# Kernel optimization log

Hardware: AMD Instinct MI355X
Metric: run time of the kernel (lower is better)

Reference implementation:

```python
import jax, jax.numpy as jnp
import numpy as np

B, N, D_ROI = 16, 128, 12544   # images, detections/image, C*roi*roi = 256*7*7
HID, PARTS = 128, 22
DTH, CTH = 50.0, 0.8           # dist / cosine thresholds
EPS = 1e-12


def setup_inputs() -> dict:
    key = jax.random.key(0)
    ks = jax.random.split(key, 6)
    d_in = D_ROI + 2
    fv = jax.random.normal(ks[0], (B, N, D_ROI), jnp.float32)
    ctr = jax.random.uniform(ks[1], (B, N, 2), jnp.float32) * 640.0  # xyxyn*640 centers
    W1 = jax.random.normal(ks[2], (d_in, HID), jnp.float32) / np.float32(np.sqrt(d_in))
    b1 = jnp.zeros((HID,), jnp.float32)
    W2 = jax.random.normal(ks[3], (HID, HID), jnp.float32) / np.float32(np.sqrt(HID))
    b2 = jnp.zeros((HID,), jnp.float32)
    Wc = jax.random.normal(ks[4], (HID, PARTS), jnp.float32) / np.float32(np.sqrt(HID))
    bc = jnp.zeros((PARTS,), jnp.float32)
    return {"fv": fv, "ctr": ctr, "W1": W1, "b1": b1, "W2": W2, "b2": b2, "Wc": Wc, "bc": bc}


def _adjacency(fv, ctr):
    """Per-image graph build: (cdist < dth) | (cosine > cth), + PyG self-loop."""
    # squared pairwise distance (compare against DTH^2; avoids sqrt at 0)
    d2 = jnp.sum((ctr[:, :, None, :] - ctr[:, None, :, :]) ** 2, axis=-1)  # [B,N,N]
    fvn = fv / jnp.maximum(jnp.linalg.norm(fv, axis=-1, keepdims=True), EPS)
    cos = jnp.einsum("bnd,bmd->bnm", fvn, fvn)                              # [B,N,N]
    A = ((d2 < DTH * DTH) | (cos > CTH)).astype(jnp.float32)
    # GCNConv(add_self_loops=True) adds weight-1 self loops on top of existing edges
    A = A + jnp.eye(N, dtype=jnp.float32)
    deg = jnp.sum(A, axis=-1)                                               # >= 2 on diag
    dinv = jax.lax.rsqrt(deg)
    return dinv[:, :, None] * A * dinv[:, None, :]                          # D^-1/2 A D^-1/2


def reference(fv, ctr, W1, b1, W2, b2, Wc, bc):
    A_hat = _adjacency(fv, ctr)                         # [B,N,N]
    x = jnp.concatenate([fv, ctr], axis=-1)             # [B,N,D_roi+2]
    h = jax.nn.relu(jnp.einsum("bnm,bmh->bnh", A_hat, x @ W1) + b1)
    h = jax.nn.relu(jnp.einsum("bnm,bmh->bnh", A_hat, h @ W2) + b2)
    hg = jnp.mean(h, axis=1)                            # global_mean_pool per image
    logits = hg @ Wc + bc                               # [B, PARTS]
    return logits
```

## Files before the change

kernel.cpp:

```cpp
#include <hip/hip_runtime.h>
#include <stdint.h>

#define DROI   12544
#define BIMG   16
#define NDET   128
#define NHID   128

typedef __bf16 bf16x8 __attribute__((ext_vector_type(8)));
typedef float  f32x4  __attribute__((ext_vector_type(4)));

__device__ __forceinline__ unsigned pk2(float a, float b){
  unsigned ua = __float_as_uint(a), ub = __float_as_uint(b);
  ua = (ua + 0x7fffu + ((ua >> 16) & 1u)) >> 16;
  ub = (ub + 0x7fffu + ((ub >> 16) & 1u)) >> 16;
  return ua | (ub << 16);
}
__device__ __forceinline__ unsigned short bf1(float a){
  unsigned ua = __float_as_uint(a);
  return (unsigned short)((ua + 0x7fffu + ((ua >> 16) & 1u)) >> 16);
}
__device__ __forceinline__ f32x4 mfma16(bf16x8 a, bf16x8 b, f32x4 c){
  return __builtin_amdgcn_mfma_f32_16x16x32_bf16(a, b, c, 0, 0, 0);
}
__device__ __forceinline__ void gl_lds16(const void* g, void* l){
  __builtin_amdgcn_global_load_lds(
      (const __attribute__((address_space(1))) unsigned int*)g,
      (__attribute__((address_space(3))) unsigned int*)l, 16, 0, 0);
}
__device__ __forceinline__ bf16x8 ldfrag128(const short* base, int row, int bo){
  const char* p = (const char*)base + row * 128 + (bo ^ ((row & 7) << 4));
  return *(const bf16x8*)p;
}
__device__ __forceinline__ bf16x8 ldfrag256(const short* base, int row, int bo){
  const char* p = (const char*)base + row * 256 + (bo ^ ((row & 7) << 4));
  return *(const bf16x8*)p;
}

__global__ __launch_bounds__(256) void k0_wt(const float* __restrict__ W1,
                                             unsigned short* __restrict__ Wt){
  __shared__ float tile[64][133];
  const int t  = threadIdx.x;
  const int k0 = blockIdx.x * 64;
  const int r0 = t >> 5;
  const int c4 = (t & 31) * 4;
#pragma unroll
  for (int i = 0; i < 8; ++i){
    int r = r0 + i * 8;
    float4 v = *(const float4*)(W1 + (long)(k0 + r) * NHID + c4);
    tile[r][c4+0] = v.x; tile[r][c4+1] = v.y; tile[r][c4+2] = v.z; tile[r][c4+3] = v.w;
  }
  __syncthreads();
  const int h  = t >> 1;
  const int kc = (t & 1) * 32;
  unsigned* dst = (unsigned*)(Wt + (long)h * DROI + k0 + kc);
#pragma unroll
  for (int kk = 0; kk < 32; kk += 2)
    dst[kk >> 1] = pk2(tile[kc + kk][h], tile[kc + kk + 1][h]);
}

template<int SK>
__global__ __launch_bounds__(256, 2) void k1_main(const float* __restrict__ fv,
    const unsigned short* __restrict__ Wt, float* __restrict__ part){
  constexpr int KC = DROI / SK;
  constexpr int NT = KC / 64;
  __shared__ __align__(16) short lsA[2][8192];
  __shared__ __align__(16) short lsB[2][8192];
  const int tid  = threadIdx.x;
  const int wave = tid >> 6, lane = tid & 63;
  const int s = blockIdx.x, b = blockIdx.y;
  const int kbase = s * KC;

  f32x4 acc[4][8];
  {
    f32x4 z = {0.f, 0.f, 0.f, 0.f};
#pragma unroll
    for (int m = 0; m < 4; ++m)
#pragma unroll
      for (int c = 0; c < 8; ++c) acc[m][c] = z;
  }

  const int r0   = tid >> 4;
  const int colf = (tid & 15) * 4;
  const float* fvt = fv + (long)(b * NDET + r0) * DROI + kbase + colf;
  const int hh  = lane >> 3;
  const int seg = (lane & 7) ^ hh;

  float4 stg[8];
#pragma unroll
  for (int j = 0; j < 4; ++j){
    int call = wave * 4 + j;
    int h = call * 8 + hh;
    const char* g = (const char*)Wt + (long)h * (DROI * 2) + (long)kbase * 2 + seg * 16;
    gl_lds16(g, (char*)lsB[0] + call * 1024);
  }
#pragma unroll
  for (int i = 0; i < 8; ++i) stg[i] = *(const float4*)(fvt + (long)i * 16 * DROI);
  {
    char* basep = (char*)lsA[0];
#pragma unroll
    for (int i = 0; i < 8; ++i){
      int r = r0 + i * 16;
      uint2 w; w.x = pk2(stg[i].x, stg[i].y); w.y = pk2(stg[i].z, stg[i].w);
      *(uint2*)(basep + r * 128 + ((colf * 2) ^ ((r & 7) << 4))) = w;
    }
  }
  __syncthreads();

  const int outw = wave >> 1;
  const int mh   = wave & 1;
  const int lq   = lane & 15;
  int buf = 0;
  for (int t = 0; t < NT; ++t){
    const int nt = t + 1;
    if (nt < NT){
#pragma unroll
      for (int j = 0; j < 4; ++j){
        int call = wave * 4 + j;
        int h = call * 8 + hh;
        const char* g = (const char*)Wt + (long)h * (DROI * 2)
                      + (long)(kbase + nt * 64) * 2 + seg * 16;
        gl_lds16(g, (char*)lsB[buf ^ 1] + call * 1024);
      }
      const float* fp = fvt + nt * 64;
#pragma unroll
      for (int i = 0; i < 8; ++i) stg[i] = *(const float4*)(fp + (long)i * 16 * DROI);
    }
    const short* A  = lsA[buf];
    const short* Bs = outw ? lsB[buf] : lsA[buf];
#pragma unroll
    for (int kk = 0; kk < 2; ++kk){
      const int bo = kk * 64 + (lane >> 4) * 16;
      bf16x8 am[4];
#pragma unroll
      for (int m = 0; m < 4; ++m)
        am[m] = ldfrag128(A, mh * 64 + m * 16 + lq, bo);
#pragma unroll
      for (int cb = 0; cb < 8; ++cb){
        bf16x8 bb = ldfrag128(Bs, cb * 16 + lq, bo);
#pragma unroll
        for (int m = 0; m < 4; ++m)
          acc[m][cb] = mfma16(am[m], bb, acc[m][cb]);
      }
    }
    if (nt < NT){
      char* basep = (char*)lsA[buf ^ 1];
#pragma unroll
      for (int i = 0; i < 8; ++i){
        int r = r0 + i * 16;
        uint2 w; w.x = pk2(stg[i].x, stg[i].y); w.y = pk2(stg[i].z, stg[i].w);
        *(uint2*)(basep + r * 128 + ((colf * 2) ^ ((r & 7) << 4))) = w;
      }
    }
    __syncthreads();
    buf ^= 1;
  }

  float* dst = part + ((long)s * 32 + b * 2 + outw) * 16384;
#pragma unroll
  for (int m = 0; m < 4; ++m){
    const int R0 = mh * 64 + m * 16 + (lane >> 4) * 4;
#pragma unroll
    for (int cb = 0; cb < 8; ++cb){
#pragma unroll
      for (int i = 0; i < 4; ++i)
        dst[(R0 + i) * 128 + cb * 16 + lq] = acc[m][cb][i];
    }
  }
}

template<int SK>
__global__ __launch_bounds__(256) void k_reduce(const float4* __restrict__ part4,
                                                float4* __restrict__ fin4){
  const int e = blockIdx.x * 256 + threadIdx.x;
  float4 s = {0.f, 0.f, 0.f, 0.f};
#pragma unroll
  for (int k = 0; k < SK; ++k){
    float4 p = part4[(long)k * 131072 + e];
    s.x += p.x; s.y += p.y; s.z += p.z; s.w += p.w;
  }
  fin4[e] = s;
}

__global__ __launch_bounds__(256, 1) void k2f(const float* __restrict__ fin,
    const float* __restrict__ ctr, const float* __restrict__ W1,
    const float* __restrict__ b1, const float* __restrict__ W2,
    const float* __restrict__ b2, const float* __restrict__ Wc,
    const float* __restrict__ bc, float* __restrict__ out){
  __shared__ __align__(16) short Ah[16384];
  __shared__ __align__(16) short Bu[16384];
  __shared__ __align__(16) short Cu[16384];
  __shared__ float sm2[256];
  const int b   = blockIdx.x;
  const int tid = threadIdx.x;
  const float* G = fin + (long)b * 32768;
  const float* Y = G + 16384;

  if (tid < 128){
    float g = G[tid * 129];
    sm2[tid] = 1.0f / fmaxf(sqrtf(g), 1e-12f);
  }
  __syncthreads();

  const int   i   = tid >> 1;
  const int   jb  = (tid & 1) * 64;
  const float invni = sm2[i];
  const float cxi = ctr[(b * 128 + i) * 2 + 0];
  const float cyi = ctr[(b * 128 + i) * 2 + 1];
  unsigned m0 = 0, m1 = 0;
  int degloc = 0;
  for (int j4 = 0; j4 < 64; j4 += 4){
    float4 g4 = *(const float4*)(G + i * 128 + jb + j4);
    float gg[4] = {g4.x, g4.y, g4.z, g4.w};
#pragma unroll
    for (int u = 0; u < 4; ++u){
      int j = jb + j4 + u;
      float cs = gg[u] * invni * sm2[j];
      float dx = cxi - ctr[(b * 128 + j) * 2 + 0];
      float dy = cyi - ctr[(b * 128 + j) * 2 + 1];
      float d2 = dx * dx + dy * dy;
      if (d2 < 2500.0f || cs > 0.8f){
        int bp = j4 + u;
        if (bp < 32) m0 |= (1u << bp); else m1 |= (1u << (bp - 32));
        ++degloc;
      }
    }
  }
  if (i >= jb && i < jb + 64) ++degloc;
  int degfull = degloc + __shfl_xor(degloc, 1);
  if ((tid & 1) == 0) sm2[128 + i] = rsqrtf((float)degfull);
  __syncthreads();

  {
    const float dinvi = sm2[128 + i];
    char* AhB = (char*)Ah;
    for (int jp = 0; jp < 64; jp += 2){
      int j0 = jb + jp, j1 = j0 + 1;
      float a0 = (((jp   < 32) ? ((m0 >> jp)       & 1u) : ((m1 >> (jp - 32))     & 1u)) ? 1.f : 0.f);
      float a1 = (((jp+1 < 32) ? ((m0 >> (jp + 1)) & 1u) : ((m1 >> (jp + 1 - 32)) & 1u)) ? 1.f : 0.f);
      if (i == j0) a0 += 1.f;
      if (i == j1) a1 += 1.f;
      float v0 = dinvi * a0 * sm2[128 + j0];
      float v1 = dinvi * a1 * sm2[128 + j1];
      int bo = j0 * 2;
      *(unsigned*)(AhB + i * 256 + (bo ^ ((i & 7) << 4))) = pk2(v0, v1);
    }
  }

  const int c     = tid & 127;
  const int khalf = tid >> 7;
  {
    char* WB = (char*)Cu;
    for (int k8 = khalf * 64; k8 < khalf * 64 + 64; k8 += 8){
      float f[8];
#pragma unroll
      for (int u = 0; u < 8; ++u) f[u] = W2[(k8 + u) * 128 + c];
      uint4 w;
      w.x = pk2(f[0], f[1]); w.y = pk2(f[2], f[3]);
      w.z = pk2(f[4], f[5]); w.w = pk2(f[6], f[7]);
      int bo = k8 * 2;
      *(uint4*)(WB + c * 256 + (bo ^ ((c & 7) << 4))) = w;
    }
  }
  {
    const float w1a = W1[(long)12544 * NHID + c];
    const float w1b = W1[(long)12545 * NHID + c];
    char* YtB = (char*)Bu;
    for (int k8 = khalf * 64; k8 < khalf * 64 + 64; k8 += 8){
      float f[8];
#pragma unroll
      for (int u = 0; u < 8; ++u){
        int k = k8 + u;
        f[u] = Y[k * 128 + c] + ctr[(b*128 + k)*2 + 0] * w1a + ctr[(b*128 + k)*2 + 1] * w1b;
      }
      uint4 w;
      w.x = pk2(f[0], f[1]); w.y = pk2(f[2], f[3]);
      w.z = pk2(f[4], f[5]); w.w = pk2(f[6], f[7]);
      int bo = k8 * 2;
      *(uint4*)(YtB + c * 256 + (bo ^ ((c & 7) << 4))) = w;
    }
  }
  __syncthreads();

  const int wave = tid >> 6, lane = tid & 63;
  const int lq = lane & 15;
  f32x4 acc[2][8];
  f32x4 z4 = {0.f, 0.f, 0.f, 0.f};

#pragma unroll
  for (int r = 0; r < 2; ++r)
#pragma unroll
    for (int cc = 0; cc < 8; ++cc) acc[r][cc] = z4;
#pragma unroll
  for (int ks = 0; ks < 4; ++ks){
    const int bo = ks * 64 + (lane >> 4) * 16;
    bf16x8 a0 = ldfrag256(Ah, (wave*2+0)*16 + lq, bo);
    bf16x8 a1 = ldfrag256(Ah, (wave*2+1)*16 + lq, bo);
#pragma unroll
    for (int cb = 0; cb < 8; ++cb){
      bf16x8 bb = ldfrag256(Bu, cb*16 + lq, bo);
      acc[0][cb] = mfma16(a0, bb, acc[0][cb]);
      acc[1][cb] = mfma16(a1, bb, acc[1][cb]);
    }
  }
  __syncthreads();
  {
    char* BuB = (char*)Bu;
#pragma unroll
    for (int rb = 0; rb < 2; ++rb){
      const int R0 = wave*32 + rb*16 + (lane >> 4)*4;
#pragma unroll
      for (int cb = 0; cb < 8; ++cb){
        const int C = cb*16 + lq;
        const float bb1 = b1[C];
#pragma unroll
        for (int u = 0; u < 4; ++u){
          float v = fmaxf(acc[rb][cb][u] + bb1, 0.f);
          int row = R0 + u;
          *(unsigned short*)(BuB + row * 256 + ((C * 2) ^ ((row & 7) << 4))) = bf1(v);
        }
      }
    }
  }
  __syncthreads();

#pragma unroll
  for (int r = 0; r < 2; ++r)
#pragma unroll
    for (int cc = 0; cc < 8; ++cc) acc[r][cc] = z4;
#pragma unroll
  for (int ks = 0; ks < 4; ++ks){
    const int bo = ks * 64 + (lane >> 4) * 16;
    bf16x8 a0 = ldfrag256(Bu, (wave*2+0)*16 + lq, bo);
    bf16x8 a1 = ldfrag256(Bu, (wave*2+1)*16 + lq, bo);
#pragma unroll
    for (int cb = 0; cb < 8; ++cb){
      bf16x8 bb = ldfrag256(Cu, cb*16 + lq, bo);
      acc[0][cb] = mfma16(a0, bb, acc[0][cb]);
      acc[1][cb] = mfma16(a1, bb, acc[1][cb]);
    }
  }
  __syncthreads();
  {
    char* BuB = (char*)Bu;
#pragma unroll
    for (int rb = 0; rb < 2; ++rb){
      const int R0 = wave*32 + rb*16 + (lane >> 4)*4;
#pragma unroll
      for (int cb = 0; cb < 8; ++cb){
        const int C = cb*16 + lq;
#pragma unroll
        for (int u = 0; u < 4; ++u){
          int k = R0 + u;
          *(unsigned short*)(BuB + C * 256 + ((k * 2) ^ ((C & 7) << 4))) = bf1(acc[rb][cb][u]);
        }
      }
    }
  }
  __syncthreads();

#pragma unroll
  for (int r = 0; r < 2; ++r)
#pragma unroll
    for (int cc = 0; cc < 8; ++cc) acc[r][cc] = z4;
#pragma unroll
  for (int ks = 0; ks < 4; ++ks){
    const int bo = ks * 64 + (lane >> 4) * 16;
    bf16x8 a0 = ldfrag256(Ah, (wave*2+0)*16 + lq, bo);
    bf16x8 a1 = ldfrag256(Ah, (wave*2+1)*16 + lq, bo);
#pragma unroll
    for (int cb = 0; cb < 8; ++cb){
      bf16x8 bb = ldfrag256(Bu, cb*16 + lq, bo);
      acc[0][cb] = mfma16(a0, bb, acc[0][cb]);
      acc[1][cb] = mfma16(a1, bb, acc[1][cb]);
    }
  }
  float colp[8];
#pragma unroll
  for (int cb = 0; cb < 8; ++cb){
    const int C = cb*16 + lq;
    const float bb2 = b2[C];
    float sum = 0.f;
#pragma unroll
    for (int rb = 0; rb < 2; ++rb)
#pragma unroll
      for (int u = 0; u < 4; ++u)
        sum += fmaxf(acc[rb][cb][u] + bb2, 0.f);
    colp[cb] = sum;
  }
#pragma unroll
  for (int cb = 0; cb < 8; ++cb){
    float v = colp[cb];
    v += __shfl_xor(v, 16);
    v += __shfl_xor(v, 32);
    colp[cb] = v;
  }
  __syncthreads();
  float* hgp = (float*)Cu;
  if ((lane >> 4) == 0){
#pragma unroll
    for (int cb = 0; cb < 8; ++cb)
      hgp[wave * 128 + cb * 16 + lane] = colp[cb];
  }
  __syncthreads();
  float* hg = hgp + 512;
  if (tid < 128)
    hg[tid] = (hgp[tid] + hgp[128 + tid] + hgp[256 + tid] + hgp[384 + tid]) * (1.0f / 128.0f);
  __syncthreads();
  if (tid < 22){
    float a2 = bc[tid];
    for (int h = 0; h < 128; ++h) a2 += hg[h] * Wc[h * 22 + tid];
    out[b * 22 + tid] = a2;
  }
}

extern "C" void kernel_launch(void* const* d_in, const int* in_sizes, int n_in,
                              void* d_out, int out_size, void* d_ws, size_t ws_size,
                              hipStream_t stream){
  (void)in_sizes; (void)n_in; (void)out_size;
  const float* fv  = (const float*)d_in[0];
  const float* ctr = (const float*)d_in[1];
  const float* W1  = (const float*)d_in[2];
  const float* b1  = (const float*)d_in[3];
  const float* W2  = (const float*)d_in[4];
  const float* b2  = (const float*)d_in[5];
  const float* Wc  = (const float*)d_in[6];
  const float* bc  = (const float*)d_in[7];
  char* ws = (char*)d_ws;
  float* out = (float*)d_out;

  const unsigned long SZ_WT = (unsigned long)NHID * DROI * 2;
  const unsigned long SZ_FIN = (unsigned long)BIMG * 2 * 16384 * 4;

  const unsigned long need28 = SZ_WT + 28UL * 2097152UL + SZ_FIN;
  const bool big = (ws_size >= need28);
  const int SK = big ? 28 : 14;

  unsigned short* Wt   = (unsigned short*)(ws);
  float*          part = (float*)(ws + SZ_WT);
  float*          fin  = (float*)(ws + SZ_WT + (unsigned long)SK * 2097152UL);

  k0_wt<<<dim3(DROI / 64), dim3(256), 0, stream>>>(W1, Wt);
  if (big){
    k1_main<28><<<dim3(28, BIMG), dim3(256), 0, stream>>>(fv, Wt, part);
    k_reduce<28><<<dim3(512), dim3(256), 0, stream>>>((const float4*)part, (float4*)fin);
  } else {
    k1_main<14><<<dim3(14, BIMG), dim3(256), 0, stream>>>(fv, Wt, part);
    k_reduce<14><<<dim3(512), dim3(256), 0, stream>>>((const float4*)part, (float4*)fin);
  }
  k2f<<<dim3(BIMG), dim3(256), 0, stream>>>(fin, ctr, W1, b1, W2, b2, Wc, bc, out);
}
```

Baseline: 70.97 us.

## Use 512-thread GEMM blocks, bf16 split-K partials, transposed Y layout in reduce

The main Gram/projection kernel moves to 512 threads per block, with each wave owning 32 rows instead of 64. fv is loaded as contiguous 64-byte row segments per thread. Split-K partials are stored packed as bf16 in the raw MFMA fragment order, which halves the partial-sum traffic. The reduce kernel unscrambles that order and writes Y transposed, so the final kernel can read rows with float4 loads and keeps centers in shared memory. The trade-off is extra bf16 rounding error in the partial sums before they are accumulated, which could affect the cosine-threshold adjacency decisions.

Result: faster. 65.35 us (-7.9%).

```diff
diff --git a/kernel.cpp b/kernel.cpp
--- a/kernel.cpp
+++ b/kernel.cpp
@@ -59,8 +59,8 @@
 }
 
 template<int SK>
-__global__ __launch_bounds__(256, 2) void k1_main(const float* __restrict__ fv,
-    const unsigned short* __restrict__ Wt, float* __restrict__ part){
+__global__ __launch_bounds__(512, 4) void k1_main(const float* __restrict__ fv,
+    const unsigned short* __restrict__ Wt, unsigned* __restrict__ part){
   constexpr int KC = DROI / SK;
   constexpr int NT = KC / 64;
   __shared__ __align__(16) short lsA[2][8192];
@@ -70,52 +70,54 @@
   const int s = blockIdx.x, b = blockIdx.y;
   const int kbase = s * KC;
 
-  f32x4 acc[4][8];
+  f32x4 acc[2][8];
   {
     f32x4 z = {0.f, 0.f, 0.f, 0.f};
 #pragma unroll
-    for (int m = 0; m < 4; ++m)
+    for (int m = 0; m < 2; ++m)
 #pragma unroll
       for (int c = 0; c < 8; ++c) acc[m][c] = z;
   }
 
-  const int r0   = tid >> 4;
-  const int colf = (tid & 15) * 4;
+  const int r0   = tid >> 2;
+  const int colf = (tid & 3) * 16;
   const float* fvt = fv + (long)(b * NDET + r0) * DROI + kbase + colf;
   const int hh  = lane >> 3;
   const int seg = (lane & 7) ^ hh;
 
-  float4 stg[8];
-#pragma unroll
-  for (int j = 0; j < 4; ++j){
-    int call = wave * 4 + j;
+  float4 stg[4];
+#pragma unroll
+  for (int j = 0; j < 2; ++j){
+    int call = wave * 2 + j;
     int h = call * 8 + hh;
     const char* g = (const char*)Wt + (long)h * (DROI * 2) + (long)kbase * 2 + seg * 16;
     gl_lds16(g, (char*)lsB[0] + call * 1024);
   }
 #pragma unroll
-  for (int i = 0; i < 8; ++i) stg[i] = *(const float4*)(fvt + (long)i * 16 * DROI);
+  for (int i = 0; i < 4; ++i) stg[i] = *(const float4*)(fvt + i * 4);
   {
     char* basep = (char*)lsA[0];
-#pragma unroll
-    for (int i = 0; i < 8; ++i){
-      int r = r0 + i * 16;
-      uint2 w; w.x = pk2(stg[i].x, stg[i].y); w.y = pk2(stg[i].z, stg[i].w);
-      *(uint2*)(basep + r * 128 + ((colf * 2) ^ ((r & 7) << 4))) = w;
-    }
-  }
-  __syncthreads();
-
-  const int outw = wave >> 1;
-  const int mh   = wave & 1;
+    uint4 w0, w1;
+    w0.x = pk2(stg[0].x, stg[0].y); w0.y = pk2(stg[0].z, stg[0].w);
+    w0.z = pk2(stg[1].x, stg[1].y); w0.w = pk2(stg[1].z, stg[1].w);
+    w1.x = pk2(stg[2].x, stg[2].y); w1.y = pk2(stg[2].z, stg[2].w);
+    w1.z = pk2(stg[3].x, stg[3].y); w1.w = pk2(stg[3].z, stg[3].w);
+    const int bo = colf * 2, sw = (r0 & 7) << 4;
+    *(uint4*)(basep + r0 * 128 + (bo ^ sw)) = w0;
+    *(uint4*)(basep + r0 * 128 + ((bo + 16) ^ sw)) = w1;
+  }
+  __syncthreads();
+
+  const int outw = wave >> 2;
+  const int mq   = wave & 3;
   const int lq   = lane & 15;
   int buf = 0;
   for (int t = 0; t < NT; ++t){
     const int nt = t + 1;
     if (nt < NT){
 #pragma unroll
-      for (int j = 0; j < 4; ++j){
-        int call = wave * 4 + j;
+      for (int j = 0; j < 2; ++j){
+        int call = wave * 2 + j;
         int h = call * 8 + hh;
         const char* g = (const char*)Wt + (long)h * (DROI * 2)
                       + (long)(kbase + nt * 64) * 2 + seg * 16;
@@ -123,62 +125,81 @@
       }
       const float* fp = fvt + nt * 64;
 #pragma unroll
-      for (int i = 0; i < 8; ++i) stg[i] = *(const float4*)(fp + (long)i * 16 * DROI);
+      for (int i = 0; i < 4; ++i) stg[i] = *(const float4*)(fp + i * 4);
     }
     const short* A  = lsA[buf];
     const short* Bs = outw ? lsB[buf] : lsA[buf];
 #pragma unroll
     for (int kk = 0; kk < 2; ++kk){
       const int bo = kk * 64 + (lane >> 4) * 16;
-      bf16x8 am[4];
-#pragma unroll
-      for (int m = 0; m < 4; ++m)
-        am[m] = ldfrag128(A, mh * 64 + m * 16 + lq, bo);
+      bf16x8 a0 = ldfrag128(A, mq * 32 + lq, bo);
+      bf16x8 a1 = ldfrag128(A, mq * 32 + 16 + lq, bo);
 #pragma unroll
       for (int cb = 0; cb < 8; ++cb){
         bf16x8 bb = ldfrag128(Bs, cb * 16 + lq, bo);
-#pragma unroll
-        for (int m = 0; m < 4; ++m)
-          acc[m][cb] = mfma16(am[m], bb, acc[m][cb]);
+        acc[0][cb] = mfma16(a0, bb, acc[0][cb]);
+        acc[1][cb] = mfma16(a1, bb, acc[1][cb]);
       }
     }
     if (nt < NT){
       char* basep = (char*)lsA[buf ^ 1];
-#pragma unroll
-      for (int i = 0; i < 8; ++i){
-        int r = r0 + i * 16;
-        uint2 w; w.x = pk2(stg[i].x, stg[i].y); w.y = pk2(stg[i].z, stg[i].w);
-        *(uint2*)(basep + r * 128 + ((colf * 2) ^ ((r & 7) << 4))) = w;
-      }
+      uint4 w0, w1;
+      w0.x = pk2(stg[0].x, stg[0].y); w0.y = pk2(stg[0].z, stg[0].w);
+      w0.z = pk2(stg[1].x, stg[1].y); w0.w = pk2(stg[1].z, stg[1].w);
+      w1.x = pk2(stg[2].x, stg[2].y); w1.y = pk2(stg[2].z, stg[2].w);
+      w1.z = pk2(stg[3].x, stg[3].y); w1.w = pk2(stg[3].z, stg[3].w);
+      const int bo = colf * 2, sw = (r0 & 7) << 4;
+      *(uint4*)(basep + r0 * 128 + (bo ^ sw)) = w0;
+      *(uint4*)(basep + r0 * 128 + ((bo + 16) ^ sw)) = w1;
     }
     __syncthreads();
     buf ^= 1;
   }
 
-  float* dst = part + ((long)s * 32 + b * 2 + outw) * 16384;
-#pragma unroll
-  for (int m = 0; m < 4; ++m){
-    const int R0 = mh * 64 + m * 16 + (lane >> 4) * 4;
-#pragma unroll
-    for (int cb = 0; cb < 8; ++cb){
-#pragma unroll
-      for (int i = 0; i < 4; ++i)
-        dst[(R0 + i) * 128 + cb * 16 + lq] = acc[m][cb][i];
-    }
+  const int slot = mq * 64 + lane;
+  uint4* dst4 = (uint4*)(part + (((long)s * 32 + b * 2 + outw) * 8192));
+#pragma unroll
+  for (int g = 0; g < 8; ++g){
+    const int m = g >> 2, cb0 = (g & 3) * 2;
+    uint4 w;
+    w.x = pk2(acc[m][cb0][0],     acc[m][cb0][1]);
+    w.y = pk2(acc[m][cb0][2],     acc[m][cb0][3]);
+    w.z = pk2(acc[m][cb0 + 1][0], acc[m][cb0 + 1][1]);
+    w.w = pk2(acc[m][cb0 + 1][2], acc[m][cb0 + 1][3]);
+    dst4[g * 256 + slot] = w;
   }
 }
 
 template<int SK>
-__global__ __launch_bounds__(256) void k_reduce(const float4* __restrict__ part4,
-                                                float4* __restrict__ fin4){
-  const int e = blockIdx.x * 256 + threadIdx.x;
-  float4 s = {0.f, 0.f, 0.f, 0.f};
-#pragma unroll
-  for (int k = 0; k < SK; ++k){
-    float4 p = part4[(long)k * 131072 + e];
-    s.x += p.x; s.y += p.y; s.z += p.z; s.w += p.w;
-  }
-  fin4[e] = s;
+__global__ __launch_bounds__(256) void k_reduce(const unsigned* __restrict__ part,
+                                                float* __restrict__ fin){
+  const int gq   = blockIdx.x * 256 + threadIdx.x;
+  const int q    = gq & 8191;
+  const int bo2  = gq >> 13;
+  float lo = 0.f, hi = 0.f;
+#pragma unroll
+  for (int s = 0; s < SK; ++s){
+    unsigned v = part[(long)s * 262144 + (long)bo2 * 8192 + q];
+    lo += __uint_as_float(v << 16);
+    hi += __uint_as_float(v & 0xffff0000u);
+  }
+  const int g    = q >> 10;
+  const int slot = (q & 1023) >> 2;
+  const int w    = q & 3;
+  const int m  = g >> 2;
+  const int cb = (g & 3) * 2 + (w >> 1);
+  const int ip = w & 1;
+  const int mq = slot >> 6, lane = slot & 63;
+  const int R = mq * 32 + m * 16 + (lane >> 4) * 4 + ip * 2;
+  const int C = cb * 16 + (lane & 15);
+  float* f = fin + (long)bo2 * 16384;
+  if ((bo2 & 1) == 0){
+    f[R * 128 + C] = lo;
+    f[(R + 1) * 128 + C] = hi;
+  } else {
+    float2 v2; v2.x = lo; v2.y = hi;
+    *(float2*)(f + C * 128 + R) = v2;
+  }
 }
 
 __global__ __launch_bounds__(256, 1) void k2f(const float* __restrict__ fin,
@@ -190,11 +211,13 @@
   __shared__ __align__(16) short Bu[16384];
   __shared__ __align__(16) short Cu[16384];
   __shared__ float sm2[256];
+  __shared__ float sctr[256];
   const int b   = blockIdx.x;
   const int tid = threadIdx.x;
-  const float* G = fin + (long)b * 32768;
-  const float* Y = G + 16384;
-
+  const float* G  = fin + (long)b * 32768;
+  const float* Yt = G + 16384;
+
+  sctr[tid] = ctr[b * 256 + tid];
   if (tid < 128){
     float g = G[tid * 129];
     sm2[tid] = 1.0f / fmaxf(sqrtf(g), 1e-12f);
@@ -204,8 +227,7 @@
   const int   i   = tid >> 1;
   const int   jb  = (tid & 1) * 64;
   const float invni = sm2[i];
-  const float cxi = ctr[(b * 128 + i) * 2 + 0];
-  const float cyi = ctr[(b * 128 + i) * 2 + 1];
+  const float cxi = sctr[2 * i], cyi = sctr[2 * i + 1];
   unsigned m0 = 0, m1 = 0;
   int degloc = 0;
   for (int j4 = 0; j4 < 64; j4 += 4){
@@ -215,8 +237,8 @@
     for (int u = 0; u < 4; ++u){
       int j = jb + j4 + u;
       float cs = gg[u] * invni * sm2[j];
-      float dx = cxi - ctr[(b * 128 + j) * 2 + 0];
-      float dy = cyi - ctr[(b * 128 + j) * 2 + 1];
+      float dx = cxi - sctr[2 * j];
+      float dy = cyi - sctr[2 * j + 1];
       float d2 = dx * dx + dy * dy;
       if (d2 < 2500.0f || cs > 0.8f){
         int bp = j4 + u;
@@ -246,9 +268,9 @@
     }
   }
 
-  const int c     = tid & 127;
-  const int khalf = tid >> 7;
-  {
+  {
+    const int c     = tid & 127;
+    const int khalf = tid >> 7;
     char* WB = (char*)Cu;
     for (int k8 = khalf * 64; k8 < khalf * 64 + 64; k8 += 8){
       float f[8];
@@ -262,21 +284,26 @@
     }
   }
   {
-    const float w1a = W1[(long)12544 * NHID + c];
-    const float w1b = W1[(long)12545 * NHID + c];
+    const int cr = tid >> 1;
+    const int kh = (tid & 1) * 64;
+    const float w1a = W1[(long)12544 * NHID + cr];
+    const float w1b = W1[(long)12545 * NHID + cr];
+    const float* Yr = Yt + cr * 128 + kh;
     char* YtB = (char*)Bu;
-    for (int k8 = khalf * 64; k8 < khalf * 64 + 64; k8 += 8){
-      float f[8];
+    for (int k8 = 0; k8 < 64; k8 += 8){
+      float4 va = *(const float4*)(Yr + k8);
+      float4 vb = *(const float4*)(Yr + k8 + 4);
+      float f[8] = {va.x, va.y, va.z, va.w, vb.x, vb.y, vb.z, vb.w};
 #pragma unroll
       for (int u = 0; u < 8; ++u){
-        int k = k8 + u;
-        f[u] = Y[k * 128 + c] + ctr[(b*128 + k)*2 + 0] * w1a + ctr[(b*128 + k)*2 + 1] * w1b;
+        int k = kh + k8 + u;
+        f[u] += sctr[2 * k] * w1a + sctr[2 * k + 1] * w1b;
       }
       uint4 w;
       w.x = pk2(f[0], f[1]); w.y = pk2(f[2], f[3]);
       w.z = pk2(f[4], f[5]); w.w = pk2(f[6], f[7]);
-      int bo = k8 * 2;
-      *(uint4*)(YtB + c * 256 + (bo ^ ((c & 7) << 4))) = w;
+      int bo = (kh + k8) * 2;
+      *(uint4*)(YtB + cr * 256 + (bo ^ ((cr & 7) << 4))) = w;
     }
   }
   __syncthreads();
@@ -428,24 +455,24 @@
   char* ws = (char*)d_ws;
   float* out = (float*)d_out;
 
-  const unsigned long SZ_WT = (unsigned long)NHID * DROI * 2;
+  const unsigned long SZ_WT  = (unsigned long)NHID * DROI * 2;
   const unsigned long SZ_FIN = (unsigned long)BIMG * 2 * 16384 * 4;
 
-  const unsigned long need28 = SZ_WT + 28UL * 2097152UL + SZ_FIN;
+  const unsigned long need28 = SZ_WT + 28UL * 1048576UL + SZ_FIN;
   const bool big = (ws_size >= need28);
   const int SK = big ? 28 : 14;
 
   unsigned short* Wt   = (unsigned short*)(ws);
-  float*          part = (float*)(ws + SZ_WT);
-  float*          fin  = (float*)(ws + SZ_WT + (unsigned long)SK * 2097152UL);
+  unsigned*       part = (unsigned*)(ws + SZ_WT);
+  float*          fin  = (float*)(ws + SZ_WT + (unsigned long)SK * 1048576UL);
 
   k0_wt<<<dim3(DROI / 64), dim3(256), 0, stream>>>(W1, Wt);
   if (big){
-    k1_main<28><<<dim3(28, BIMG), dim3(256), 0, stream>>>(fv, Wt, part);
-    k_reduce<28><<<dim3(512), dim3(256), 0, stream>>>((const float4*)part, (float4*)fin);
+    k1_main<28><<<dim3(28, BIMG), dim3(512), 0, stream>>>(fv, Wt, part);
+    k_reduce<28><<<dim3(1024), dim3(256), 0, stream>>>(part, fin);
   } else {
-    k1_main<14><<<dim3(14, BIMG), dim3(256), 0, stream>>>(fv, Wt, part);
-    k_reduce<14><<<dim3(512), dim3(256), 0, stream>>>((const float4*)part, (float4*)fin);
+    k1_main<14><<<dim3(14, BIMG), dim3(512), 0, stream>>>(fv, Wt, part);
+    k_reduce<14><<<dim3(1024), dim3(256), 0, stream>>>(part, fin);
   }
   k2f<<<dim3(BIMG), dim3(256), 0, stream>>>(fin, ctr, W1, b1, W2, b2, Wc, bc, out);
 }
```
